# Performance work log

Measured on AMD Instinct MI355X. Metric: run time of the kernel, lower is better.

Reference implementation:

```python
import jax, jax.numpy as jnp
import numpy as np

B, L, D, H = 2, 2048, 1024, 16
DH = D // H  # 64


def setup_inputs() -> dict:
    key = jax.random.key(0)
    ks = jax.random.split(key, 9)
    s = 1.0 / np.sqrt(D)
    x = jax.random.normal(ks[0], (B, L, D), dtype=jnp.float32)
    # per-head projection weights stacked on leading head axis (torch Linear: y = x W^T + b)
    Wq = jax.random.normal(ks[1], (H, D, DH), dtype=jnp.float32) * s
    bq = jax.random.normal(ks[2], (H, DH), dtype=jnp.float32) * s
    Wk = jax.random.normal(ks[3], (H, D, DH), dtype=jnp.float32) * s
    bk = jax.random.normal(ks[4], (H, DH), dtype=jnp.float32) * s
    Wv = jax.random.normal(ks[5], (H, D, DH), dtype=jnp.float32) * s
    bv = jax.random.normal(ks[6], (H, DH), dtype=jnp.float32) * s
    WO = jax.random.normal(ks[7], (D, D), dtype=jnp.float32) * s  # torch layout [out, in]
    bO = jax.random.normal(ks[8], (D,), dtype=jnp.float32) * s
    return {"x": x, "Wq": Wq, "bq": bq, "Wk": Wk, "bk": bk,
            "Wv": Wv, "bv": bv, "WO": WO, "bO": bO}


def reference(x, Wq, bq, Wk, bk, Wv, bv, WO, bO):
    # Q,K,V: [B,H,L,DH]
    Q = jnp.einsum('bld,hdk->bhlk', x, Wq) + bq[None, :, None, :]
    K = jnp.einsum('bld,hdk->bhlk', x, Wk) + bk[None, :, None, :]
    V = jnp.einsum('bld,hdk->bhlk', x, Wv) + bv[None, :, None, :]
    scale = 1.0 / jnp.sqrt(jnp.asarray(DH, dtype=x.dtype))
    att = jnp.einsum('bhik,bhjk->bhij', Q, K) * scale  # [B,H,Lq,Lk]
    # NOTE: original softmaxes over dim=1 of [B,Lq,Lk] -> the QUERY axis (axis=2 here)
    att = jax.nn.softmax(att, axis=2)
    # dropout is identity in eval/reference mode
    out = jnp.einsum('bhij,bhjk->bhik', att, V)  # [B,H,L,DH]
    out = out.transpose(0, 2, 1, 3).reshape(B, L, D)  # concat heads on feature axis
    return jnp.einsum('bld,ed->ble', out, WO) + bO
```

## Files before the change

kernel.cpp:

```cpp
#include <hip/hip_runtime.h>
#include <math.h>

#define NB 2
#define NL 2048
#define ND 1024
#define NH 16
#define NDH 64
static constexpr float SCALE = 0.125f;

typedef short          bhalf8 __attribute__((ext_vector_type(8)));
typedef unsigned short ush8   __attribute__((ext_vector_type(8)));
typedef unsigned short ush4   __attribute__((ext_vector_type(4)));
typedef float          f32x4  __attribute__((ext_vector_type(4)));

#define MFMA_BF16(a, b, c) __builtin_amdgcn_mfma_f32_16x16x32_bf16(a, b, c, 0, 0, 0)

__device__ __forceinline__ unsigned short f2bf(float f) {
    unsigned u = __float_as_uint(f);
    u += 0x7FFF + ((u >> 16) & 1);
    return (unsigned short)(u >> 16);
}
__device__ __forceinline__ float bf2f(unsigned short s) {
    return __uint_as_float((unsigned)s << 16);
}
__device__ __forceinline__ unsigned pack_bf16(float lo, float hi) {
    unsigned a = __float_as_uint(lo) + 0x8000u;
    unsigned b = __float_as_uint(hi) + 0x8000u;
    return __builtin_amdgcn_perm(b, a, 0x07060302u);
}
__device__ __forceinline__ void gload16(const unsigned short* g, unsigned short* l) {
    __builtin_amdgcn_global_load_lds(
        (const __attribute__((address_space(1))) unsigned int*)(const void*)g,
        (__attribute__((address_space(3))) unsigned int*)(void*)l,
        16, 0, 0);
}

__global__ __launch_bounds__(256) void k_cvt(
    const float* __restrict__ x, const float* __restrict__ WO,
    unsigned short* __restrict__ xb, unsigned short* __restrict__ wob)
{
    size_t u = (size_t)blockIdx.x * 256 + threadIdx.x;
    const float* src; unsigned short* dst; size_t off;
    if (u < 524288) { src = x;  dst = xb;  off = u * 8; }
    else            { src = WO; dst = wob; off = (u - 524288) * 8; }
    float4 a = *(const float4*)(src + off);
    float4 b = *(const float4*)(src + off + 4);
    uint4 o;
    o.x = pack_bf16(a.x, a.y); o.y = pack_bf16(a.z, a.w);
    o.z = pack_bf16(b.x, b.y); o.w = pack_bf16(b.z, b.w);
    *(uint4*)(dst + off) = o;
}

__global__ __launch_bounds__(256) void k_cvt_wt(
    const float* __restrict__ Wq, const float* __restrict__ Wk,
    const float* __restrict__ Wv, unsigned short* __restrict__ Wtb)
{
    __shared__ unsigned short T[64][72];
    const int d0  = blockIdx.x * 64;
    const int qkv = blockIdx.y >> 4;
    const int h   = blockIdx.y & 15;
    const float* W = (qkv == 0 ? Wq : (qkv == 1 ? Wk : Wv)) + (size_t)h * (ND * NDH);
    const int t = threadIdx.x;
#pragma unroll
    for (int p = 0; p < 4; ++p) {
        int u  = t + p * 256;
        int dr = u >> 4;
        int c4 = (u & 15) * 4;
        float4 v = *(const float4*)(W + (size_t)(d0 + dr) * NDH + c4);
        T[c4 + 0][dr] = f2bf(v.x);
        T[c4 + 1][dr] = f2bf(v.y);
        T[c4 + 2][dr] = f2bf(v.z);
        T[c4 + 3][dr] = f2bf(v.w);
    }
    __syncthreads();
    unsigned short* outp = Wtb + (size_t)(qkv * NH + h) * NDH * ND;
#pragma unroll
    for (int p = 0; p < 2; ++p) {
        int u  = t + p * 256;
        int dh = u >> 3;
        int sg = (u & 7) * 8;
        *(ush8*)(outp + (size_t)dh * ND + d0 + sg) = *(ush8*)&T[dh][sg];
    }
}

__global__ __launch_bounds__(256, 2) void k_qkv_mfma(
    const unsigned short* __restrict__ xb, const unsigned short* __restrict__ Wtb,
    const float* __restrict__ bq, const float* __restrict__ bk,
    const float* __restrict__ bv,
    unsigned short* __restrict__ Qb, unsigned short* __restrict__ Kb,
    unsigned short* __restrict__ Vtb)
{
    __shared__ unsigned short LB[2 * 128 * 64];
    unsigned short* As = LB;
    unsigned short* Bs = LB + 128 * 64;

    const int mt = blockIdx.x;
    const int nt = blockIdx.y;
    const int qkv = nt >> 3;
    const int t = threadIdx.x, w = t >> 6, lane = t & 63;
    const int lr = lane & 15, lg = lane >> 4;
    const int wm = (w >> 1) * 64, wn = (w & 1) * 64;
    const int swz = (lr & 7) << 3;
    const int rA = lane >> 3, cg = (lane & 7) * 8;

    f32x4 acc[4][4] = {};

    for (int k0 = 0; k0 < ND; k0 += 64) {
        __syncthreads();
#pragma unroll
        for (int i = 0; i < 4; ++i) {
            int c  = w * 4 + i;
            int r  = c * 8 + rA;
            int gc = cg ^ ((r & 7) << 3);
            gload16(xb  + (size_t)(mt * 128 + r) * ND + k0 + gc, &As[c * 512]);
            gload16(Wtb + (size_t)(nt * 128 + r) * ND + k0 + gc, &Bs[c * 512]);
        }
        __syncthreads();

        bhalf8 av[4][2], bw[4][2];
#pragma unroll
        for (int f = 0; f < 4; ++f)
#pragma unroll
            for (int ks = 0; ks < 2; ++ks) {
                int c = (ks * 32 + lg * 8) ^ swz;
                av[f][ks] = *(const bhalf8*)&As[(wm + f * 16 + lr) * 64 + c];
                bw[f][ks] = *(const bhalf8*)&Bs[(wn + f * 16 + lr) * 64 + c];
            }
#pragma unroll
        for (int mf = 0; mf < 4; ++mf)
#pragma unroll
            for (int nf = 0; nf < 4; ++nf) {
                acc[mf][nf] = MFMA_BF16(av[mf][0], bw[nf][0], acc[mf][nf]);
                acc[mf][nf] = MFMA_BF16(av[mf][1], bw[nf][1], acc[mf][nf]);
            }
    }

    const float* bias = (qkv == 0 ? bq : (qkv == 1 ? bk : bv));
    const int nb = (nt & 7) * 128;
    float bi[4];
#pragma unroll
    for (int nf = 0; nf < 4; ++nf) bi[nf] = bias[nb + wn + nf * 16 + lr];

    __syncthreads();
    unsigned short* TS = LB;

    if (qkv < 2) {
#pragma unroll
        for (int mf = 0; mf < 4; ++mf)
#pragma unroll
            for (int nf = 0; nf < 4; ++nf)
#pragma unroll
                for (int r = 0; r < 4; ++r) {
                    int m = wm + mf * 16 + lg * 4 + r;
                    int n = (wn + nf * 16 + lr) ^ ((m & 7) << 3);
                    TS[m * 128 + n] = f2bf(acc[mf][nf][r] + bi[nf]);
                }
        __syncthreads();
        unsigned short* outp = (qkv == 0 ? Qb : Kb);
#pragma unroll
        for (int p = 0; p < 8; ++p) {
            int u = t + p * 256;
            int r = u >> 4, sg = (u & 15) * 8;
            ush8 v = *(const ush8*)&TS[r * 128 + (sg ^ ((r & 7) << 3))];
            int m = mt * 128 + r;
            int b = m >> 11, l = m & (NL - 1);
            int n = nb + sg;
            int h = n >> 6, dh = n & 63;
            *(ush8*)(outp + ((size_t)(b * NH + h) * NL + l) * NDH + dh) = v;
        }
    } else {
#pragma unroll
        for (int mf = 0; mf < 4; ++mf)
#pragma unroll
            for (int nf = 0; nf < 4; ++nf) {
                int n = wn + nf * 16 + lr;
                int mc = (wm + mf * 16 + lg * 4) ^ ((n & 7) << 3);
                ush4 pk;
#pragma unroll
                for (int r = 0; r < 4; ++r) pk[r] = f2bf(acc[mf][nf][r] + bi[nf]);
                *(ush4*)&TS[n * 128 + mc] = pk;
            }
        __syncthreads();
#pragma unroll
        for (int p = 0; p < 8; ++p) {
            int u = t + p * 256;
            int r = u >> 4, sg = (u & 15) * 8;
            ush8 v = *(const ush8*)&TS[r * 128 + (sg ^ ((r & 7) << 3))];
            int n = nb + r;
            int h = n >> 6, dh = n & 63;
            int m0 = mt * 128 + sg;
            int b = m0 >> 11, l0 = m0 & (NL - 1);
            *(ush8*)(Vtb + ((size_t)(b * NH + h) * NDH + dh) * NL + l0) = v;
        }
    }
}

__global__ __launch_bounds__(512, 4) void k_colsum_mfma(
    const unsigned short* __restrict__ Qb, const unsigned short* __restrict__ Kb,
    unsigned short* __restrict__ Vtb)
{
    __shared__ unsigned short Ks[128 * 64];
    __shared__ unsigned short Qs[64 * 64];
    __shared__ float rzbuf[128];

    const int jt = blockIdx.x;
    const int bh = blockIdx.y;
    const unsigned short* Qp = Qb + (size_t)bh * NL * NDH;
    const unsigned short* Kp = Kb + (size_t)bh * NL * NDH;
    const int t = threadIdx.x, w = t >> 6, lane = t & 63;
    const int lr = lane & 15, lg = lane >> 4;
    const int wj = w * 16;
    const int swz = (lr & 7) << 3;
    const int rA = lane >> 3, cg = (lane & 7) * 8;

#pragma unroll
    for (int i = 0; i < 2; ++i) {
        int c  = w * 2 + i;
        int r  = c * 8 + rA;
        int gc = cg ^ ((r & 7) << 3);
        gload16(Kp + (size_t)(jt * 128 + r) * NDH + gc, &Ks[c * 512]);
    }

    float zacc[4] = {};

    for (int it = 0; it < 32; ++it) {
        __syncthreads();
        {
            int r  = w * 8 + rA;
            int gc = cg ^ ((r & 7) << 3);
            gload16(Qp + (size_t)(it * 64 + r) * NDH + gc, &Qs[w * 512]);
        }
        __syncthreads();

        bhalf8 ka[2];
#pragma unroll
        for (int ks = 0; ks < 2; ++ks)
            ka[ks] = *(const bhalf8*)&Ks[(wj + lr) * 64 + ((ks * 32 + lg * 8) ^ swz)];
#pragma unroll
        for (int ii = 0; ii < 4; ++ii) {
            bhalf8 q0 = *(const bhalf8*)&Qs[(ii * 16 + lr) * 64 + ((lg * 8) ^ swz)];
            bhalf8 q1 = *(const bhalf8*)&Qs[(ii * 16 + lr) * 64 + ((32 + lg * 8) ^ swz)];
            f32x4 s = {};
            s = MFMA_BF16(ka[0], q0, s);
            s = MFMA_BF16(ka[1], q1, s);
#pragma unroll
            for (int r = 0; r < 4; ++r) zacc[r] += __expf(s[r] * SCALE);
        }
    }

#pragma unroll
    for (int r = 0; r < 4; ++r) {
        float v = zacc[r];
        v += __shfl_xor(v, 1);
        v += __shfl_xor(v, 2);
        v += __shfl_xor(v, 4);
        v += __shfl_xor(v, 8);
        if (lr == 0) rzbuf[wj + lg * 4 + r] = 1.0f / v;
    }
    __syncthreads();

    unsigned short* Vp = Vtb + (size_t)bh * NDH * NL + jt * 128;
    {
        int dh = t >> 3, jj = (t & 7) * 16;
        unsigned short* vp = Vp + (size_t)dh * NL + jj;
        ush8 v0 = *(const ush8*)vp;
        ush8 v1 = *(const ush8*)(vp + 8);
        float4 z0 = *(const float4*)&rzbuf[jj];
        float4 z1 = *(const float4*)&rzbuf[jj + 4];
        float4 z2 = *(const float4*)&rzbuf[jj + 8];
        float4 z3 = *(const float4*)&rzbuf[jj + 12];
        uint4 o0, o1;
        o0.x = pack_bf16(bf2f(v0[0]) * z0.x, bf2f(v0[1]) * z0.y);
        o0.y = pack_bf16(bf2f(v0[2]) * z0.z, bf2f(v0[3]) * z0.w);
        o0.z = pack_bf16(bf2f(v0[4]) * z1.x, bf2f(v0[5]) * z1.y);
        o0.w = pack_bf16(bf2f(v0[6]) * z1.z, bf2f(v0[7]) * z1.w);
        o1.x = pack_bf16(bf2f(v1[0]) * z2.x, bf2f(v1[1]) * z2.y);
        o1.y = pack_bf16(bf2f(v1[2]) * z2.z, bf2f(v1[3]) * z2.w);
        o1.z = pack_bf16(bf2f(v1[4]) * z3.x, bf2f(v1[5]) * z3.y);
        o1.w = pack_bf16(bf2f(v1[6]) * z3.z, bf2f(v1[7]) * z3.w);
        *(uint4*)vp = o0;
        *(uint4*)(vp + 8) = o1;
    }
}

__global__ __launch_bounds__(512, 4) void k_av_mfma(
    const unsigned short* __restrict__ Qb, const unsigned short* __restrict__ Kb,
    const unsigned short* __restrict__ Vtb, unsigned short* __restrict__ AOb)
{
    __shared__ unsigned short Qs[128 * 64];
    __shared__ unsigned short Ks[64 * 64];
    __shared__ unsigned short Vts[64 * 64];
    __shared__ unsigned short Ps[128 * 64];

    const int it = blockIdx.x;
    const int bh = blockIdx.y;
    const int b = bh >> 4, h = bh & 15;
    const unsigned short* Qp = Qb  + (size_t)bh * NL * NDH;
    const unsigned short* Kp = Kb  + (size_t)bh * NL * NDH;
    const unsigned short* Vp = Vtb + (size_t)bh * NDH * NL;

    const int t = threadIdx.x, w = t >> 6, lane = t & 63;
    const int lr = lane & 15, lg = lane >> 4;
    const int wi = w * 16;
    const int swz = (lr & 7) << 3;
    const int rA = lane >> 3, cg = (lane & 7) * 8;

#pragma unroll
    for (int i = 0; i < 2; ++i) {
        int c  = w * 2 + i;
        int r  = c * 8 + rA;
        int gc = cg ^ ((r & 7) << 3);
        gload16(Qp + (size_t)(it * 128 + r) * NDH + gc, &Qs[c * 512]);
    }

    f32x4 oacc[4] = {};

    for (int jt = 0; jt < 32; ++jt) {
        __syncthreads();
        {
            int r  = w * 8 + rA;
            int gc = cg ^ ((r & 7) << 3);
            gload16(Kp + (size_t)(jt * 64 + r) * NDH + gc, &Ks[w * 512]);
            gload16(Vp + (size_t)r * NL + jt * 64 + gc,    &Vts[w * 512]);
        }
        __syncthreads();

        bhalf8 qa[2];
#pragma unroll
        for (int ks = 0; ks < 2; ++ks)
            qa[ks] = *(const bhalf8*)&Qs[(wi + lr) * 64 + ((ks * 32 + lg * 8) ^ swz)];
#pragma unroll
        for (int jf = 0; jf < 4; ++jf) {
            bhalf8 k0v = *(const bhalf8*)&Ks[(jf * 16 + lr) * 64 + ((lg * 8) ^ swz)];
            bhalf8 k1v = *(const bhalf8*)&Ks[(jf * 16 + lr) * 64 + ((32 + lg * 8) ^ swz)];
            f32x4 s = {};
            s = MFMA_BF16(k0v, qa[0], s);
            s = MFMA_BF16(k1v, qa[1], s);
            uint2 pk;
            pk.x = pack_bf16(__expf(s[0] * SCALE), __expf(s[1] * SCALE));
            pk.y = pack_bf16(__expf(s[2] * SCALE), __expf(s[3] * SCALE));
            *(uint2*)&Ps[(wi + lr) * 64 + ((jf * 16 + lg * 4) ^ swz)] = pk;
        }

        bhalf8 pa[2];
#pragma unroll
        for (int ks = 0; ks < 2; ++ks)
            pa[ks] = *(const bhalf8*)&Ps[(wi + lr) * 64 + ((ks * 32 + lg * 8) ^ swz)];
#pragma unroll
        for (int nf = 0; nf < 4; ++nf) {
            bhalf8 v0 = *(const bhalf8*)&Vts[(nf * 16 + lr) * 64 + ((lg * 8) ^ swz)];
            bhalf8 v1 = *(const bhalf8*)&Vts[(nf * 16 + lr) * 64 + ((32 + lg * 8) ^ swz)];
            oacc[nf] = MFMA_BF16(pa[0], v0, oacc[nf]);
            oacc[nf] = MFMA_BF16(pa[1], v1, oacc[nf]);
        }
    }

    __syncthreads();
#pragma unroll
    for (int nf = 0; nf < 4; ++nf)
#pragma unroll
        for (int r = 0; r < 4; ++r) {
            int li  = wi + lg * 4 + r;
            int dhc = (nf * 16 + lr) ^ ((li & 7) << 3);
            Ps[li * 64 + dhc] = f2bf(oacc[nf][r]);
        }
    __syncthreads();
    {
        int r = t >> 2, sgq = (t & 3) * 16;
        int sz2 = (r & 7) << 3;
        ush8 v0 = *(const ush8*)&Ps[r * 64 + (sgq ^ sz2)];
        ush8 v1 = *(const ush8*)&Ps[r * 64 + ((sgq + 8) ^ sz2)];
        unsigned short* op = AOb + ((size_t)(b * NL + it * 128 + r)) * ND + h * NDH + sgq;
        *(ush8*)op = v0;
        *(ush8*)(op + 8) = v1;
    }
}

__global__ __launch_bounds__(256, 2) void k_oproj_mfma(
    const unsigned short* __restrict__ AOb, const unsigned short* __restrict__ WOb,
    const float* __restrict__ bO, float* __restrict__ y)
{
    __shared__ unsigned short As[64 * 64];
    __shared__ unsigned short Bs[128 * 64];

    const int mt = blockIdx.x;
    const int nt = blockIdx.y;
    const int t = threadIdx.x, w = t >> 6, lane = t & 63;
    const int lr = lane & 15, lg = lane >> 4;
    const int wn = w * 32;
    const int swz = (lr & 7) << 3;
    const int rA = lane >> 3, cg = (lane & 7) * 8;

    f32x4 acc[4][2] = {};

    for (int k0 = 0; k0 < ND; k0 += 64) {
        __syncthreads();
#pragma unroll
        for (int i = 0; i < 2; ++i) {
            int c  = w * 2 + i;
            int r  = c * 8 + rA;
            int gc = cg ^ ((r & 7) << 3);
            gload16(AOb + (size_t)(mt * 64 + r) * ND + k0 + gc, &As[c * 512]);
        }
#pragma unroll
        for (int i = 0; i < 4; ++i) {
            int c  = w * 4 + i;
            int r  = c * 8 + rA;
            int gc = cg ^ ((r & 7) << 3);
            gload16(WOb + (size_t)(nt * 128 + r) * ND + k0 + gc, &Bs[c * 512]);
        }
        __syncthreads();

        bhalf8 bw[2][2];
#pragma unroll
        for (int nf = 0; nf < 2; ++nf)
#pragma unroll
            for (int ks = 0; ks < 2; ++ks)
                bw[nf][ks] = *(const bhalf8*)&Bs[(wn + nf * 16 + lr) * 64 +
                                                ((ks * 32 + lg * 8) ^ swz)];
#pragma unroll
        for (int mf = 0; mf < 4; ++mf) {
            bhalf8 a0 = *(const bhalf8*)&As[(mf * 16 + lr) * 64 + ((lg * 8) ^ swz)];
            bhalf8 a1 = *(const bhalf8*)&As[(mf * 16 + lr) * 64 + ((32 + lg * 8) ^ swz)];
#pragma unroll
            for (int nf = 0; nf < 2; ++nf) {
                acc[mf][nf] = MFMA_BF16(a0, bw[nf][0], acc[mf][nf]);
                acc[mf][nf] = MFMA_BF16(a1, bw[nf][1], acc[mf][nf]);
            }
        }
    }

#pragma unroll
    for (int mf = 0; mf < 4; ++mf)
#pragma unroll
        for (int nf = 0; nf < 2; ++nf) {
            int e = nt * 128 + wn + nf * 16 + lr;
            float bo = bO[e];
#pragma unroll
            for (int r = 0; r < 4; ++r) {
                int m = mt * 64 + mf * 16 + lg * 4 + r;
                y[(size_t)m * ND + e] = acc[mf][nf][r] + bo;
            }
        }
}

extern "C" void kernel_launch(void* const* d_in, const int* in_sizes, int n_in,
                              void* d_out, int out_size, void* d_ws, size_t ws_size,
                              hipStream_t stream)
{
    const float* x  = (const float*)d_in[0];
    const float* Wq = (const float*)d_in[1];
    const float* bq = (const float*)d_in[2];
    const float* Wk = (const float*)d_in[3];
    const float* bk = (const float*)d_in[4];
    const float* Wv = (const float*)d_in[5];
    const float* bv = (const float*)d_in[6];
    const float* WO = (const float*)d_in[7];
    const float* bO = (const float*)d_in[8];
    float* y = (float*)d_out;

    unsigned short* xb  = (unsigned short*)d_ws;
    unsigned short* Wtb = xb  + 4194304;
    unsigned short* WOb = Wtb + 3145728;
    unsigned short* Qb  = WOb + 1048576;
    unsigned short* Kb  = Qb  + 4194304;
    unsigned short* Vtb = Kb  + 4194304;
    unsigned short* AOb = Vtb + 4194304;

    hipLaunchKernelGGL(k_cvt,         dim3(2560),   dim3(256), 0, stream, x, WO, xb, WOb);
    hipLaunchKernelGGL(k_cvt_wt,      dim3(16, 48), dim3(256), 0, stream, Wq, Wk, Wv, Wtb);
    hipLaunchKernelGGL(k_qkv_mfma,    dim3(32, 24), dim3(256), 0, stream,
                       xb, Wtb, bq, bk, bv, Qb, Kb, Vtb);
    hipLaunchKernelGGL(k_colsum_mfma, dim3(16, 32), dim3(512), 0, stream, Qb, Kb, Vtb);
    hipLaunchKernelGGL(k_av_mfma,     dim3(16, 32), dim3(512), 0, stream, Qb, Kb, Vtb, AOb);
    hipLaunchKernelGGL(k_oproj_mfma,  dim3(64, 8),  dim3(256), 0, stream, AOb, WOb, bO, y);
}
```

Measured before the change: 215.7 us.

## Retile colsum and AV attention kernels into 2D warp tiles with register-held fragments

```diff
diff --git a/kernel.cpp b/kernel.cpp
--- a/kernel.cpp
+++ b/kernel.cpp
@@ -195,12 +195,13 @@
     }
 }
 
-__global__ __launch_bounds__(512, 4) void k_colsum_mfma(
+__global__ __launch_bounds__(512) void k_colsum_mfma(
     const unsigned short* __restrict__ Qb, const unsigned short* __restrict__ Kb,
     unsigned short* __restrict__ Vtb)
 {
     __shared__ unsigned short Ks[128 * 64];
     __shared__ unsigned short Qs[64 * 64];
+    __shared__ float zpart[2][128];
     __shared__ float rzbuf[128];
 
     const int jt = blockIdx.x;
@@ -209,7 +210,8 @@
     const unsigned short* Kp = Kb + (size_t)bh * NL * NDH;
     const int t = threadIdx.x, w = t >> 6, lane = t & 63;
     const int lr = lane & 15, lg = lane >> 4;
-    const int wj = w * 16;
+    const int jg = w & 3;
+    const int ig = w >> 2;
     const int swz = (lr & 7) << 3;
     const int rA = lane >> 3, cg = (lane & 7) * 8;
 
@@ -220,8 +222,16 @@
         int gc = cg ^ ((r & 7) << 3);
         gload16(Kp + (size_t)(jt * 128 + r) * NDH + gc, &Ks[c * 512]);
     }
-
-    float zacc[4] = {};
+    __syncthreads();
+    bhalf8 kf[2][2];
+#pragma unroll
+    for (int jf = 0; jf < 2; ++jf)
+#pragma unroll
+        for (int ks = 0; ks < 2; ++ks)
+            kf[jf][ks] = *(const bhalf8*)&Ks[(jg * 32 + jf * 16 + lr) * 64 +
+                                            ((ks * 32 + lg * 8) ^ swz)];
+
+    float zacc[2][4] = {};
 
     for (int it = 0; it < 32; ++it) {
         __syncthreads();
@@ -232,31 +242,34 @@
         }
         __syncthreads();
 
-        bhalf8 ka[2];
-#pragma unroll
-        for (int ks = 0; ks < 2; ++ks)
-            ka[ks] = *(const bhalf8*)&Ks[(wj + lr) * 64 + ((ks * 32 + lg * 8) ^ swz)];
-#pragma unroll
-        for (int ii = 0; ii < 4; ++ii) {
-            bhalf8 q0 = *(const bhalf8*)&Qs[(ii * 16 + lr) * 64 + ((lg * 8) ^ swz)];
-            bhalf8 q1 = *(const bhalf8*)&Qs[(ii * 16 + lr) * 64 + ((32 + lg * 8) ^ swz)];
-            f32x4 s = {};
-            s = MFMA_BF16(ka[0], q0, s);
-            s = MFMA_BF16(ka[1], q1, s);
-#pragma unroll
-            for (int r = 0; r < 4; ++r) zacc[r] += __expf(s[r] * SCALE);
-        }
-    }
-
-#pragma unroll
-    for (int r = 0; r < 4; ++r) {
-        float v = zacc[r];
-        v += __shfl_xor(v, 1);
-        v += __shfl_xor(v, 2);
-        v += __shfl_xor(v, 4);
-        v += __shfl_xor(v, 8);
-        if (lr == 0) rzbuf[wj + lg * 4 + r] = 1.0f / v;
-    }
+#pragma unroll
+        for (int ii = 0; ii < 2; ++ii) {
+            bhalf8 q0 = *(const bhalf8*)&Qs[(ig * 32 + ii * 16 + lr) * 64 + ((lg * 8) ^ swz)];
+            bhalf8 q1 = *(const bhalf8*)&Qs[(ig * 32 + ii * 16 + lr) * 64 + ((32 + lg * 8) ^ swz)];
+#pragma unroll
+            for (int jf = 0; jf < 2; ++jf) {
+                f32x4 s = {};
+                s = MFMA_BF16(kf[jf][0], q0, s);
+                s = MFMA_BF16(kf[jf][1], q1, s);
+#pragma unroll
+                for (int r = 0; r < 4; ++r) zacc[jf][r] += __expf(s[r] * SCALE);
+            }
+        }
+    }
+
+#pragma unroll
+    for (int jf = 0; jf < 2; ++jf)
+#pragma unroll
+        for (int r = 0; r < 4; ++r) {
+            float v = zacc[jf][r];
+            v += __shfl_xor(v, 1);
+            v += __shfl_xor(v, 2);
+            v += __shfl_xor(v, 4);
+            v += __shfl_xor(v, 8);
+            if (lr == 0) zpart[ig][jg * 32 + jf * 16 + lg * 4 + r] = v;
+        }
+    __syncthreads();
+    if (t < 128) rzbuf[t] = 1.0f / (zpart[0][t] + zpart[1][t]);
     __syncthreads();
 
     unsigned short* Vp = Vtb + (size_t)bh * NDH * NL + jt * 128;
@@ -283,7 +296,7 @@
     }
 }
 
-__global__ __launch_bounds__(512, 4) void k_av_mfma(
+__global__ __launch_bounds__(512) void k_av_mfma(
     const unsigned short* __restrict__ Qb, const unsigned short* __restrict__ Kb,
     const unsigned short* __restrict__ Vtb, unsigned short* __restrict__ AOb)
 {
@@ -301,7 +314,8 @@
 
     const int t = threadIdx.x, w = t >> 6, lane = t & 63;
     const int lr = lane & 15, lg = lane >> 4;
-    const int wi = w * 16;
+    const int jgS = w & 1;
+    const int igS = w >> 1;
     const int swz = (lr & 7) << 3;
     const int rA = lane >> 3, cg = (lane & 7) * 8;
 
@@ -312,8 +326,16 @@
         int gc = cg ^ ((r & 7) << 3);
         gload16(Qp + (size_t)(it * 128 + r) * NDH + gc, &Qs[c * 512]);
     }
-
-    f32x4 oacc[4] = {};
+    __syncthreads();
+    bhalf8 qf[2][2];
+#pragma unroll
+    for (int ii = 0; ii < 2; ++ii)
+#pragma unroll
+        for (int ks = 0; ks < 2; ++ks)
+            qf[ii][ks] = *(const bhalf8*)&Qs[(igS * 32 + ii * 16 + lr) * 64 +
+                                            ((ks * 32 + lg * 8) ^ swz)];
+
+    f32x4 oacc[2][4] = {};
 
     for (int jt = 0; jt < 32; ++jt) {
         __syncthreads();
@@ -325,45 +347,58 @@
         }
         __syncthreads();
 
-        bhalf8 qa[2];
-#pragma unroll
-        for (int ks = 0; ks < 2; ++ks)
-            qa[ks] = *(const bhalf8*)&Qs[(wi + lr) * 64 + ((ks * 32 + lg * 8) ^ swz)];
-#pragma unroll
-        for (int jf = 0; jf < 4; ++jf) {
-            bhalf8 k0v = *(const bhalf8*)&Ks[(jf * 16 + lr) * 64 + ((lg * 8) ^ swz)];
-            bhalf8 k1v = *(const bhalf8*)&Ks[(jf * 16 + lr) * 64 + ((32 + lg * 8) ^ swz)];
-            f32x4 s = {};
-            s = MFMA_BF16(k0v, qa[0], s);
-            s = MFMA_BF16(k1v, qa[1], s);
-            uint2 pk;
-            pk.x = pack_bf16(__expf(s[0] * SCALE), __expf(s[1] * SCALE));
-            pk.y = pack_bf16(__expf(s[2] * SCALE), __expf(s[3] * SCALE));
-            *(uint2*)&Ps[(wi + lr) * 64 + ((jf * 16 + lg * 4) ^ swz)] = pk;
-        }
-
-        bhalf8 pa[2];
-#pragma unroll
-        for (int ks = 0; ks < 2; ++ks)
-            pa[ks] = *(const bhalf8*)&Ps[(wi + lr) * 64 + ((ks * 32 + lg * 8) ^ swz)];
-#pragma unroll
-        for (int nf = 0; nf < 4; ++nf) {
-            bhalf8 v0 = *(const bhalf8*)&Vts[(nf * 16 + lr) * 64 + ((lg * 8) ^ swz)];
-            bhalf8 v1 = *(const bhalf8*)&Vts[(nf * 16 + lr) * 64 + ((32 + lg * 8) ^ swz)];
-            oacc[nf] = MFMA_BF16(pa[0], v0, oacc[nf]);
-            oacc[nf] = MFMA_BF16(pa[1], v1, oacc[nf]);
-        }
-    }
-
-    __syncthreads();
-#pragma unroll
-    for (int nf = 0; nf < 4; ++nf)
-#pragma unroll
-        for (int r = 0; r < 4; ++r) {
-            int li  = wi + lg * 4 + r;
-            int dhc = (nf * 16 + lr) ^ ((li & 7) << 3);
-            Ps[li * 64 + dhc] = f2bf(oacc[nf][r]);
-        }
+#pragma unroll
+        for (int jf = 0; jf < 2; ++jf) {
+            bhalf8 k0 = *(const bhalf8*)&Ks[(jgS * 32 + jf * 16 + lr) * 64 + ((lg * 8) ^ swz)];
+            bhalf8 k1 = *(const bhalf8*)&Ks[(jgS * 32 + jf * 16 + lr) * 64 + ((32 + lg * 8) ^ swz)];
+#pragma unroll
+            for (int ii = 0; ii < 2; ++ii) {
+                f32x4 s = {};
+                s = MFMA_BF16(k0, qf[ii][0], s);
+                s = MFMA_BF16(k1, qf[ii][1], s);
+                uint2 pk;
+                pk.x = pack_bf16(__expf(s[0] * SCALE), __expf(s[1] * SCALE));
+                pk.y = pack_bf16(__expf(s[2] * SCALE), __expf(s[3] * SCALE));
+                int i = igS * 32 + ii * 16 + lr;
+                *(uint2*)&Ps[i * 64 + ((jgS * 32 + jf * 16 + lg * 4) ^ ((i & 7) << 3))] = pk;
+            }
+        }
+        __syncthreads();
+
+        if (w < 4) {
+            bhalf8 pa[2][2];
+#pragma unroll
+            for (int iif = 0; iif < 2; ++iif)
+#pragma unroll
+                for (int ks = 0; ks < 2; ++ks)
+                    pa[iif][ks] = *(const bhalf8*)&Ps[(w * 32 + iif * 16 + lr) * 64 +
+                                                     ((ks * 32 + lg * 8) ^ swz)];
+#pragma unroll
+            for (int nf = 0; nf < 4; ++nf) {
+                bhalf8 v0 = *(const bhalf8*)&Vts[(nf * 16 + lr) * 64 + ((lg * 8) ^ swz)];
+                bhalf8 v1 = *(const bhalf8*)&Vts[(nf * 16 + lr) * 64 + ((32 + lg * 8) ^ swz)];
+#pragma unroll
+                for (int iif = 0; iif < 2; ++iif) {
+                    oacc[iif][nf] = MFMA_BF16(pa[iif][0], v0, oacc[iif][nf]);
+                    oacc[iif][nf] = MFMA_BF16(pa[iif][1], v1, oacc[iif][nf]);
+                }
+            }
+        }
+    }
+
+    __syncthreads();
+    if (w < 4) {
+#pragma unroll
+        for (int iif = 0; iif < 2; ++iif)
+#pragma unroll
+            for (int nf = 0; nf < 4; ++nf)
+#pragma unroll
+                for (int r = 0; r < 4; ++r) {
+                    int li  = w * 32 + iif * 16 + lg * 4 + r;
+                    int dhc = (nf * 16 + lr) ^ ((li & 7) << 3);
+                    Ps[li * 64 + dhc] = f2bf(oacc[iif][nf][r]);
+                }
+    }
     __syncthreads();
     {
         int r = t >> 2, sgq = (t & 3) * 16;
```

Result: no change. 215.1 us (-0.3%).
